# Performance work log

Hardware: AMD Instinct MI355X
Metric: run time of the kernel (lower is better)

## Reference

```python
import jax, jax.numpy as jnp
import numpy as np

D_MODEL = 1024
N_HEAD = 16
D_QKV = 64
B, L = 2, 2048
LN_EPS = 1e-5


def setup_inputs() -> dict:
    key = jax.random.key(0)
    ks = jax.random.split(key, 5)
    # xavier-normal-ish scale for [H, d_model, d_qkv] params
    std_in = (2.0 / (D_MODEL + D_QKV)) ** 0.5
    return {
        "x": jax.random.normal(ks[0], (B, L, D_MODEL), jnp.float32),
        "w_q": jax.random.normal(ks[1], (N_HEAD, D_MODEL, D_QKV), jnp.float32) * std_in,
        "w_k": jax.random.normal(ks[2], (N_HEAD, D_MODEL, D_QKV), jnp.float32) * std_in,
        "w_v": jax.random.normal(ks[3], (N_HEAD, D_MODEL, D_QKV), jnp.float32) * std_in,
        "w_o": jax.random.normal(ks[4], (N_HEAD, D_QKV, D_MODEL), jnp.float32) * std_in,
        "ln_gamma": jnp.ones((D_MODEL,), jnp.float32),
        "ln_beta": jnp.zeros((D_MODEL,), jnp.float32),
    }


def reference(x, w_q, w_k, w_v, w_o, ln_gamma, ln_beta):
    # q,k,v: [B, H, L, d_qkv]
    q = jnp.einsum('hmq,blm->bhlq', w_q, x)
    k = jnp.einsum('hmq,blm->bhlq', w_k, x)
    v = jnp.einsum('hmq,blm->bhlq', w_v, x)
    # scores: [B, H, L, L]
    s = jnp.einsum('bhiq,bhjq->bhij', q, k) / (D_QKV ** 0.5)
    s = jax.nn.softmax(s, axis=-1)
    # (dropout disabled: eval-mode reference)
    att = jnp.einsum('bhij,bhjq->bhiq', s, v)          # [B, H, L, d_qkv]
    out = jnp.einsum('bhlq,hqm->blm', att, w_o)        # [B, L, d_model]
    y = x + out                                        # residual
    mu = jnp.mean(y, axis=-1, keepdims=True)
    var = jnp.var(y, axis=-1, keepdims=True)
    return (y - mu) * jax.lax.rsqrt(var + LN_EPS) * ln_gamma + ln_beta
```

## Files before the change

### kernel.cpp

```cpp
#include <hip/hip_runtime.h>
#include <hip/hip_bf16.h>
#include <cstdint>

#define B_      2
#define L_      2048
#define DM_     1024
#define H_      16
#define DQ_     64
#define LN_EPS  1e-5f
#define QSCALE  0.1803368801111204f

typedef unsigned short u16;
typedef unsigned int   u32;
typedef __attribute__((ext_vector_type(8)))  short short8;
typedef __attribute__((ext_vector_type(4)))  unsigned short u16x4;
typedef __attribute__((ext_vector_type(4)))  unsigned int   u32x4;
typedef __attribute__((ext_vector_type(4)))  float f32x4;
typedef __attribute__((ext_vector_type(16))) float f32x16;

__device__ __forceinline__ u16 f2b(float f) {
  __hip_bfloat16 h = __float2bfloat16(f);
  return *reinterpret_cast<u16*>(&h);
}
__device__ __forceinline__ u32 pk2(float lo, float hi) {
  return (u32)f2b(lo) | ((u32)f2b(hi) << 16);
}

__device__ __forceinline__ void gl_lds16(const void* g, void* l) {
  auto gp = reinterpret_cast<const __attribute__((address_space(1))) unsigned int*>(
      reinterpret_cast<uintptr_t>(g));
  auto lp = reinterpret_cast<__attribute__((address_space(3))) unsigned int*>(
      reinterpret_cast<uintptr_t>(l));
  __builtin_amdgcn_global_load_lds(gp, lp, 16, 0, 0);
}

__device__ __forceinline__ short8 frag8(const u16* base, int row, int lchunk) {
  return *(const short8*)(base + row * 64 + ((lchunk ^ (row & 7)) << 3));
}

__global__ __launch_bounds__(256) void prep_all(
    const float* __restrict__ x, const float* __restrict__ wq,
    const float* __restrict__ wk, const float* __restrict__ wv,
    const float* __restrict__ wo, u16* __restrict__ xb,
    u16* __restrict__ wt, u16* __restrict__ wot) {
  __shared__ float Ls[64][65];
  const int t = threadIdx.x;
  const int bx = blockIdx.x;
  if (bx < 4096) {
    int i = bx * 256 + t;
    float4 v = ((const float4*)x)[i];
    u16x4 o = { f2b(v.x), f2b(v.y), f2b(v.z), f2b(v.w) };
    *(u16x4*)(xb + (size_t)i * 4) = o;
  } else if (bx < 4096 + 768) {
    int b2 = bx - 4096;
    int mt = b2 & 15, h = (b2 >> 4) & 15, wh = b2 >> 8;
    const float* in = ((wh == 0) ? wq : (wh == 1) ? wk : wv) + (size_t)h * DM_ * DQ_;
    #pragma unroll
    for (int i = 0; i < 16; ++i) {
      int idx = i * 256 + t, r = idx >> 6, c = idx & 63;
      Ls[r][c] = in[(size_t)(mt * 64 + r) * DQ_ + c];
    }
    __syncthreads();
    u16* outb = wt + (size_t)(wh * H_ + h) * DQ_ * DM_;
    #pragma unroll
    for (int i = 0; i < 16; ++i) {
      int idx = i * 256 + t, q = idx >> 6, mm = idx & 63;
      outb[(size_t)q * DM_ + mt * 64 + mm] = f2b(Ls[mm][q]);
    }
  } else {
    int b3 = bx - 4864;
    int mt = b3 & 15, kt = b3 >> 4;
    #pragma unroll
    for (int i = 0; i < 16; ++i) {
      int idx = i * 256 + t, r = idx >> 6, c = idx & 63;
      Ls[r][c] = wo[(size_t)(kt * 64 + r) * DM_ + mt * 64 + c];
    }
    __syncthreads();
    #pragma unroll
    for (int i = 0; i < 16; ++i) {
      int idx = i * 256 + t, mm = idx >> 6, kk = idx & 63;
      wot[(size_t)(mt * 64 + mm) * DM_ + kt * 64 + kk] = f2b(Ls[kk][mm]);
    }
  }
}

__global__ __launch_bounds__(256) void qkv_big(const u16* __restrict__ xb,
    const u16* __restrict__ wt, u16* __restrict__ Q, u16* __restrict__ K,
    u16* __restrict__ Vtg) {
  const int nt = blockIdx.x, mt = blockIdx.y;
  __shared__ __align__(16) u16 SH[128 * 136];
  u16* As_ = SH;
  u16* Bs_ = SH + 8192;
  const int t = threadIdx.x, w = t >> 6, lane = t & 63;
  const int lx = lane & 15, lq = lane >> 4;
  const int row0 = mt * 128, n0 = nt * 128;
  const int r8 = lane >> 3, lc = (lane & 7) ^ r8;
  const int wr = (w >> 1) * 64, wc = (w & 1) * 64;

  const u16* gA = xb + (size_t)(row0 + w * 32 + r8) * DM_ + lc * 8;
  const u16* gB = wt + (size_t)(n0  + w * 32 + r8) * DM_ + lc * 8;
  u16* lA = As_ + (w * 32) * 64;
  u16* lB = Bs_ + (w * 32) * 64;

  f32x4 z = {0.f, 0.f, 0.f, 0.f};
  f32x4 acc[4][4];
  #pragma unroll
  for (int mb = 0; mb < 4; ++mb)
    #pragma unroll
    for (int nb = 0; nb < 4; ++nb) acc[mb][nb] = z;

  for (int k0 = 0; k0 < DM_; k0 += 64) {
    #pragma unroll
    for (int i = 0; i < 4; ++i) {
      gl_lds16(gA + (size_t)i * 8 * DM_ + k0, lA + i * 8 * 64);
      gl_lds16(gB + (size_t)i * 8 * DM_ + k0, lB + i * 8 * 64);
    }
    __syncthreads();
    short8 af[4][2];
    #pragma unroll
    for (int mb = 0; mb < 4; ++mb)
      #pragma unroll
      for (int kh = 0; kh < 2; ++kh)
        af[mb][kh] = frag8(As_, wr + mb * 16 + lx, (kh << 2) | lq);
    #pragma unroll
    for (int nb = 0; nb < 4; ++nb) {
      short8 b0 = frag8(Bs_, wc + nb * 16 + lx, lq);
      short8 b1 = frag8(Bs_, wc + nb * 16 + lx, 4 | lq);
      #pragma unroll
      for (int mb = 0; mb < 4; ++mb) {
        acc[mb][nb] = __builtin_amdgcn_mfma_f32_16x16x32_bf16(af[mb][0], b0, acc[mb][nb], 0, 0, 0);
        acc[mb][nb] = __builtin_amdgcn_mfma_f32_16x16x32_bf16(af[mb][1], b1, acc[mb][nb], 0, 0, 0);
      }
    }
    __syncthreads();
  }

  const int wh = n0 >> 10;
  const float oscale = (wh == 0) ? QSCALE : 1.0f;
  const int bb = row0 >> 11, l0 = row0 & 2047;
  const int hd0 = n0 & 1023;
  u16* Ep = SH;

  if (wh != 2) {
    #pragma unroll
    for (int mb = 0; mb < 4; ++mb)
      #pragma unroll
      for (int nb = 0; nb < 4; ++nb)
        #pragma unroll
        for (int r = 0; r < 4; ++r) {
          int l = wr + mb * 16 + lq * 4 + r;
          Ep[l * 136 + wc + nb * 16 + lx] = f2b(acc[mb][nb][r] * oscale);
        }
    __syncthreads();
    u16* outp = (wh == 0) ? Q : K;
    #pragma unroll
    for (int hs = 0; hs < 2; ++hs) {
      const int hh = (hd0 >> 6) + hs;
      u16* gbase = outp + ((size_t)(bb * H_ + hh) * L_ + l0) * DQ_;
      #pragma unroll
      for (int it = 0; it < 4; ++it) {
        int u = it * 256 + t;
        int l = u >> 3, chunk = u & 7;
        *(uint4*)(gbase + u * 8) = *(const uint4*)&Ep[l * 136 + hs * 64 + chunk * 8];
      }
    }
  } else {
    #pragma unroll
    for (int mb = 0; mb < 4; ++mb)
      #pragma unroll
      for (int nb = 0; nb < 4; ++nb) {
        int l = wr + mb * 16 + lq * 4;
        int lp = (l & ~12) | ((l & 4) << 1) | ((l & 8) >> 1);
        uint2 pv = { pk2(acc[mb][nb][0], acc[mb][nb][1]),
                     pk2(acc[mb][nb][2], acc[mb][nb][3]) };
        *(uint2*)&Ep[(wc + nb * 16 + lx) * 136 + lp] = pv;
      }
    __syncthreads();
    #pragma unroll
    for (int it = 0; it < 8; ++it) {
      int v = it * 256 + t;
      int dloc = v >> 4, chunk = v & 15;
      int hh = (hd0 + dloc) >> 6, dd = (hd0 + dloc) & 63;
      u16* g = Vtg + ((size_t)(bb * H_ + hh) * DQ_ + dd) * L_ + l0 + chunk * 8;
      *(uint4*)g = *(const uint4*)&Ep[dloc * 136 + chunk * 8];
    }
  }
}

__global__ __launch_bounds__(512) void attn_mfma(const u16* __restrict__ Q,
    const u16* __restrict__ K, const u16* __restrict__ Vtg, u16* __restrict__ att) {
  const int qt = blockIdx.x, h = blockIdx.y, b = blockIdx.z;
  __shared__ __align__(16) u16 Qs_[256 * 64];
  __shared__ __align__(16) u16 Ks_[2][64 * 64];
  __shared__ __align__(16) u16 Vt_[2][64 * 64];
  const int t = threadIdx.x, w = t >> 6, lane = t & 63;
  const int c = lane & 31, lsel = lane >> 5;
  const int r8 = lane >> 3, lc = (lane & 7) ^ r8;
  const size_t bh  = (size_t)(b * H_ + h) * L_ * DQ_;
  const size_t bhv = (size_t)(b * H_ + h) * DQ_ * L_;

  const u16* gQ = Q + bh + (size_t)(qt * 256 + w * 32 + r8) * DQ_ + lc * 8;
  #pragma unroll
  for (int i = 0; i < 4; ++i) gl_lds16(gQ + (size_t)i * 8 * DQ_, Qs_ + (w * 32 + i * 8) * 64);

  const u16* gK = K   + bh  + (size_t)(w * 8 + r8) * DQ_ + lc * 8;
  const u16* gV = Vtg + bhv + (size_t)(w * 8 + r8) * L_  + lc * 8;

  gl_lds16(gK, Ks_[0] + w * 8 * 64);
  gl_lds16(gV, Vt_[0] + w * 8 * 64);
  __syncthreads();
  short8 qb[4];
  #pragma unroll
  for (int km = 0; km < 4; ++km) qb[km] = frag8(Qs_, w * 32 + c, (km << 1) | lsel);

  f32x16 zz = {0.f,0.f,0.f,0.f,0.f,0.f,0.f,0.f,0.f,0.f,0.f,0.f,0.f,0.f,0.f,0.f};
  f32x16 oacc0 = zz, oacc1 = zz, lacc = zz;
  const short one_bf = (short)0x3F80;
  short8 ones = {one_bf, one_bf, one_bf, one_bf, one_bf, one_bf, one_bf, one_bf};

  for (int kt = 0; kt < L_ / 64; ++kt) {
    const int cur = kt & 1;
    __syncthreads();

    if (kt + 1 < L_ / 64) {
      const int nxt = 1 - cur;
      gl_lds16(gK + (size_t)(kt + 1) * 64 * DQ_, Ks_[nxt] + w * 8 * 64);
      gl_lds16(gV + (size_t)(kt + 1) * 64,       Vt_[nxt] + w * 8 * 64);
    }

    u32x4 paw[4];
    #pragma unroll
    for (int kb = 0; kb < 2; ++kb) {
      f32x16 s = zz;
      #pragma unroll
      for (int km = 0; km < 4; ++km) {
        short8 ka = frag8(Ks_[cur], kb * 32 + c, (km << 1) | lsel);
        s = __builtin_amdgcn_mfma_f32_32x32x16_bf16(ka, qb[km], s, 0, 0, 0);
      }
      #pragma unroll
      for (int F = 0; F < 2; ++F) {
        u32x4 pw;
        #pragma unroll
        for (int i = 0; i < 4; ++i) {
          float p0 = __builtin_amdgcn_exp2f(s[8 * F + 2 * i]);
          float p1 = __builtin_amdgcn_exp2f(s[8 * F + 2 * i + 1]);
          pw[i] = __builtin_amdgcn_perm(__float_as_uint(p1), __float_as_uint(p0), 0x07060302u);
        }
        paw[2 * kb + F] = pw;
      }
    }

    #pragma unroll
    for (int km = 0; km < 4; ++km) {
      short8 pa  = *reinterpret_cast<const short8*>(&paw[km]);
      short8 vb0 = frag8(Vt_[cur], c,      (km << 1) | lsel);
      short8 vb1 = frag8(Vt_[cur], 32 + c, (km << 1) | lsel);
      oacc0 = __builtin_amdgcn_mfma_f32_32x32x16_bf16(pa, vb0, oacc0, 0, 0, 0);
      oacc1 = __builtin_amdgcn_mfma_f32_32x32x16_bf16(pa, vb1, oacc1, 0, 0, 0);
      lacc  = __builtin_amdgcn_mfma_f32_32x32x16_bf16(pa, ones, lacc, 0, 0, 0);
    }
  }

  const int qrow_base = qt * 256 + w * 32;
  #pragma unroll
  for (int r = 0; r < 16; ++r) {
    int qr = (r & 3) + 8 * (r >> 2) + 4 * lsel;
    float inv = 1.0f / lacc[r];
    size_t base = (size_t)(b * L_ + qrow_base + qr) * DM_ + h * DQ_;
    att[base + c]      = f2b(oacc0[r] * inv);
    att[base + 32 + c] = f2b(oacc1[r] * inv);
  }
}

__global__ __launch_bounds__(256) void oproj_big(const u16* __restrict__ A,
    const u16* __restrict__ wot, float* __restrict__ out) {
  const int nt = blockIdx.x, mt = blockIdx.y;
  __shared__ __align__(16) u16 As_[128 * 64];
  __shared__ __align__(16) u16 Bs_[64 * 64];
  const int t = threadIdx.x, w = t >> 6, lane = t & 63;
  const int lx = lane & 15, lq = lane >> 4;
  const int row0 = mt * 128, n0 = nt * 64;
  const int r8 = lane >> 3, lc = (lane & 7) ^ r8;

  const u16* gA = A   + (size_t)(row0 + w * 32 + r8) * DM_ + lc * 8;
  const u16* gB = wot + (size_t)(n0  + w * 16 + r8) * DM_ + lc * 8;
  u16* lA = As_ + (w * 32) * 64;
  u16* lB = Bs_ + (w * 16) * 64;

  f32x4 z = {0.f, 0.f, 0.f, 0.f};
  f32x4 acc[2][4];
  #pragma unroll
  for (int mb = 0; mb < 2; ++mb)
    #pragma unroll
    for (int nb = 0; nb < 4; ++nb) acc[mb][nb] = z;

  for (int k0 = 0; k0 < DM_; k0 += 64) {
    #pragma unroll
    for (int i = 0; i < 4; ++i)
      gl_lds16(gA + (size_t)i * 8 * DM_ + k0, lA + i * 8 * 64);
    #pragma unroll
    for (int i = 0; i < 2; ++i)
      gl_lds16(gB + (size_t)i * 8 * DM_ + k0, lB + i * 8 * 64);
    __syncthreads();
    short8 af[2][2];
    #pragma unroll
    for (int mb = 0; mb < 2; ++mb)
      #pragma unroll
      for (int kh = 0; kh < 2; ++kh)
        af[mb][kh] = frag8(As_, w * 32 + mb * 16 + lx, (kh << 2) | lq);
    #pragma unroll
    for (int nb = 0; nb < 4; ++nb) {
      short8 b0 = frag8(Bs_, nb * 16 + lx, lq);
      short8 b1 = frag8(Bs_, nb * 16 + lx, 4 | lq);
      acc[0][nb] = __builtin_amdgcn_mfma_f32_16x16x32_bf16(af[0][0], b0, acc[0][nb], 0, 0, 0);
      acc[0][nb] = __builtin_amdgcn_mfma_f32_16x16x32_bf16(af[0][1], b1, acc[0][nb], 0, 0, 0);
      acc[1][nb] = __builtin_amdgcn_mfma_f32_16x16x32_bf16(af[1][0], b0, acc[1][nb], 0, 0, 0);
      acc[1][nb] = __builtin_amdgcn_mfma_f32_16x16x32_bf16(af[1][1], b1, acc[1][nb], 0, 0, 0);
    }
    __syncthreads();
  }
  #pragma unroll
  for (int mb = 0; mb < 2; ++mb)
    #pragma unroll
    for (int nb = 0; nb < 4; ++nb)
      #pragma unroll
      for (int r = 0; r < 4; ++r) {
        int row = row0 + w * 32 + mb * 16 + lq * 4 + r;
        out[(size_t)row * DM_ + n0 + nb * 16 + lx] = acc[mb][nb][r];
      }
}

__global__ __launch_bounds__(256) void resid_ln(
    const float* __restrict__ x, const float* __restrict__ gamma,
    const float* __restrict__ beta, float* __restrict__ out) {
  const int row = blockIdx.x;
  const int t   = threadIdx.x;
  const float4* xp = (const float4*)(x   + (size_t)row * DM_);
  float4*       yp = (float4*)      (out + (size_t)row * DM_);

  float4 xv = xp[t];
  float4 av = yp[t];
  float y0 = xv.x + av.x, y1 = xv.y + av.y, y2 = xv.z + av.z, y3 = xv.w + av.w;

  float s  = y0 + y1 + y2 + y3;
  float s2 = y0 * y0 + y1 * y1 + y2 * y2 + y3 * y3;
  #pragma unroll
  for (int off = 32; off > 0; off >>= 1) {
    s  += __shfl_xor(s,  off, 64);
    s2 += __shfl_xor(s2, off, 64);
  }
  __shared__ float red[8];
  const int wave = t >> 6, lane = t & 63;
  if (lane == 0) { red[wave] = s; red[4 + wave] = s2; }
  __syncthreads();
  s  = red[0] + red[1] + red[2] + red[3];
  s2 = red[4] + red[5] + red[6] + red[7];

  const float mean = s * (1.f / DM_);
  const float var  = s2 * (1.f / DM_) - mean * mean;
  const float inv  = rsqrtf(var + LN_EPS);

  const float4 g  = ((const float4*)gamma)[t];
  const float4 bt = ((const float4*)beta)[t];
  float4 r;
  r.x = (y0 - mean) * inv * g.x + bt.x;
  r.y = (y1 - mean) * inv * g.y + bt.y;
  r.z = (y2 - mean) * inv * g.z + bt.z;
  r.w = (y3 - mean) * inv * g.w + bt.w;
  yp[t] = r;
}

extern "C" void kernel_launch(void* const* d_in, const int* in_sizes, int n_in,
                              void* d_out, int out_size, void* d_ws, size_t ws_size,
                              hipStream_t stream) {
  const float* x     = (const float*)d_in[0];
  const float* wq    = (const float*)d_in[1];
  const float* wk    = (const float*)d_in[2];
  const float* wv    = (const float*)d_in[3];
  const float* wo    = (const float*)d_in[4];
  const float* gamma = (const float*)d_in[5];
  const float* beta  = (const float*)d_in[6];
  float* out = (float*)d_out;

  char* ws = (char*)d_ws;
  u16* xb  = (u16*)ws;
  u16* Qb  = (u16*)(ws + ((size_t)8  << 20));
  u16* Kb  = (u16*)(ws + ((size_t)16 << 20));
  u16* Vtg = (u16*)(ws + ((size_t)24 << 20));
  u16* wt  = (u16*)(ws + ((size_t)32 << 20));
  u16* wot = (u16*)(ws + ((size_t)38 << 20));
  u16* att = (u16*)(ws + ((size_t)40 << 20));

  prep_all <<<5120, 256, 0, stream>>>(x, wq, wk, wv, wo, xb, wt, wot);
  qkv_big  <<<dim3(24, 32),    256, 0, stream>>>(xb, wt, Qb, Kb, Vtg);
  attn_mfma<<<dim3(L_ / 256, H_, B_), 512, 0, stream>>>(Qb, Kb, Vtg, att);
  oproj_big<<<dim3(16, 32),    256, 0, stream>>>(att, wot, out);
  resid_ln <<<B_ * L_, 256, 0, stream>>>(x, gamma, beta, out);
}
```

Before: 182.2 us.

## Halve attention block size and replace ones-MFMA row sum with VALU accumulation

The attention kernel now uses 128-query tiles with 4 waves instead of 256-query tiles with 8 waves. The grid doubles, and each wave loads two K/V rows per stage to cover the 64-row tile. The softmax denominator no longer comes from a third MFMA against a ones vector. Each lane instead sums its bf16-rounded probabilities, the two half-waves are combined with a shuffle, and the sums go through shared memory. This removes a third of the PV-stage MFMAs and a 16-register accumulator, at the cost of extra VALU adds and twice as much K/V traffic per query.

```diff
diff --git a/kernel.cpp b/kernel.cpp
--- a/kernel.cpp
+++ b/kernel.cpp
@@ -187,36 +187,38 @@
   }
 }
 
-__global__ __launch_bounds__(512) void attn_mfma(const u16* __restrict__ Q,
+__global__ __launch_bounds__(256) void attn_mfma(const u16* __restrict__ Q,
     const u16* __restrict__ K, const u16* __restrict__ Vtg, u16* __restrict__ att) {
   const int qt = blockIdx.x, h = blockIdx.y, b = blockIdx.z;
-  __shared__ __align__(16) u16 Qs_[256 * 64];
+  __shared__ __align__(16) u16 Qs_[128 * 64];
   __shared__ __align__(16) u16 Ks_[2][64 * 64];
   __shared__ __align__(16) u16 Vt_[2][64 * 64];
+  __shared__ float Qsum[4][32];
   const int t = threadIdx.x, w = t >> 6, lane = t & 63;
   const int c = lane & 31, lsel = lane >> 5;
   const int r8 = lane >> 3, lc = (lane & 7) ^ r8;
   const size_t bh  = (size_t)(b * H_ + h) * L_ * DQ_;
   const size_t bhv = (size_t)(b * H_ + h) * DQ_ * L_;
 
-  const u16* gQ = Q + bh + (size_t)(qt * 256 + w * 32 + r8) * DQ_ + lc * 8;
+  const u16* gQ = Q + bh + (size_t)(qt * 128 + w * 32 + r8) * DQ_ + lc * 8;
   #pragma unroll
   for (int i = 0; i < 4; ++i) gl_lds16(gQ + (size_t)i * 8 * DQ_, Qs_ + (w * 32 + i * 8) * 64);
 
-  const u16* gK = K   + bh  + (size_t)(w * 8 + r8) * DQ_ + lc * 8;
-  const u16* gV = Vtg + bhv + (size_t)(w * 8 + r8) * L_  + lc * 8;
-
-  gl_lds16(gK, Ks_[0] + w * 8 * 64);
-  gl_lds16(gV, Vt_[0] + w * 8 * 64);
+  const u16* gK = K   + bh  + (size_t)(w * 16 + r8) * DQ_ + lc * 8;
+  const u16* gV = Vtg + bhv + (size_t)(w * 16 + r8) * L_  + lc * 8;
+
+  gl_lds16(gK,                     Ks_[0] + (w * 16)     * 64);
+  gl_lds16(gK + (size_t)8 * DQ_,   Ks_[0] + (w * 16 + 8) * 64);
+  gl_lds16(gV,                     Vt_[0] + (w * 16)     * 64);
+  gl_lds16(gV + (size_t)8 * L_,    Vt_[0] + (w * 16 + 8) * 64);
   __syncthreads();
   short8 qb[4];
   #pragma unroll
   for (int km = 0; km < 4; ++km) qb[km] = frag8(Qs_, w * 32 + c, (km << 1) | lsel);
 
   f32x16 zz = {0.f,0.f,0.f,0.f,0.f,0.f,0.f,0.f,0.f,0.f,0.f,0.f,0.f,0.f,0.f,0.f};
-  f32x16 oacc0 = zz, oacc1 = zz, lacc = zz;
-  const short one_bf = (short)0x3F80;
-  short8 ones = {one_bf, one_bf, one_bf, one_bf, one_bf, one_bf, one_bf, one_bf};
+  f32x16 oacc0 = zz, oacc1 = zz;
+  float rsum = 0.f;
 
   for (int kt = 0; kt < L_ / 64; ++kt) {
     const int cur = kt & 1;
@@ -224,8 +226,10 @@
 
     if (kt + 1 < L_ / 64) {
       const int nxt = 1 - cur;
-      gl_lds16(gK + (size_t)(kt + 1) * 64 * DQ_, Ks_[nxt] + w * 8 * 64);
-      gl_lds16(gV + (size_t)(kt + 1) * 64,       Vt_[nxt] + w * 8 * 64);
+      gl_lds16(gK + (size_t)(kt + 1) * 64 * DQ_,                    Ks_[nxt] + (w * 16)     * 64);
+      gl_lds16(gK + (size_t)((kt + 1) * 64 + 8) * DQ_,              Ks_[nxt] + (w * 16 + 8) * 64);
+      gl_lds16(gV + (size_t)(kt + 1) * 64,                          Vt_[nxt] + (w * 16)     * 64);
+      gl_lds16(gV + (size_t)8 * L_ + (size_t)(kt + 1) * 64,         Vt_[nxt] + (w * 16 + 8) * 64);
     }
 
     u32x4 paw[4];
@@ -237,6 +241,7 @@
         short8 ka = frag8(Ks_[cur], kb * 32 + c, (km << 1) | lsel);
         s = __builtin_amdgcn_mfma_f32_32x32x16_bf16(ka, qb[km], s, 0, 0, 0);
       }
+      float tp[8];
       #pragma unroll
       for (int F = 0; F < 2; ++F) {
         u32x4 pw;
@@ -244,10 +249,15 @@
         for (int i = 0; i < 4; ++i) {
           float p0 = __builtin_amdgcn_exp2f(s[8 * F + 2 * i]);
           float p1 = __builtin_amdgcn_exp2f(s[8 * F + 2 * i + 1]);
-          pw[i] = __builtin_amdgcn_perm(__float_as_uint(p1), __float_as_uint(p0), 0x07060302u);
+          u32 pkd = __builtin_amdgcn_perm(__float_as_uint(p1), __float_as_uint(p0), 0x07060302u);
+          pw[i] = pkd;
+          float t0 = __uint_as_float(pkd << 16);
+          float t1 = __uint_as_float(pkd & 0xFFFF0000u);
+          tp[4 * F + i] = t0 + t1;
         }
         paw[2 * kb + F] = pw;
       }
+      rsum += ((tp[0] + tp[1]) + (tp[2] + tp[3])) + ((tp[4] + tp[5]) + (tp[6] + tp[7]));
     }
 
     #pragma unroll
@@ -257,15 +267,18 @@
       short8 vb1 = frag8(Vt_[cur], 32 + c, (km << 1) | lsel);
       oacc0 = __builtin_amdgcn_mfma_f32_32x32x16_bf16(pa, vb0, oacc0, 0, 0, 0);
       oacc1 = __builtin_amdgcn_mfma_f32_32x32x16_bf16(pa, vb1, oacc1, 0, 0, 0);
-      lacc  = __builtin_amdgcn_mfma_f32_32x32x16_bf16(pa, ones, lacc, 0, 0, 0);
-    }
-  }
-
-  const int qrow_base = qt * 256 + w * 32;
+    }
+  }
+
+  rsum += __shfl_xor(rsum, 32, 64);
+  if (lane < 32) Qsum[w][lane] = rsum;
+  __syncthreads();
+
+  const int qrow_base = qt * 128 + w * 32;
   #pragma unroll
   for (int r = 0; r < 16; ++r) {
     int qr = (r & 3) + 8 * (r >> 2) + 4 * lsel;
-    float inv = 1.0f / lacc[r];
+    float inv = 1.0f / Qsum[w][qr];
     size_t base = (size_t)(b * L_ + qrow_base + qr) * DM_ + h * DQ_;
     att[base + c]      = f2b(oacc0[r] * inv);
     att[base + 32 + c] = f2b(oacc1[r] * inv);
@@ -393,7 +406,7 @@
 
   prep_all <<<5120, 256, 0, stream>>>(x, wq, wk, wv, wo, xb, wt, wot);
   qkv_big  <<<dim3(24, 32),    256, 0, stream>>>(xb, wt, Qb, Kb, Vtg);
-  attn_mfma<<<dim3(L_ / 256, H_, B_), 512, 0, stream>>>(Qb, Kb, Vtg, att);
+  attn_mfma<<<dim3(L_ / 128, H_, B_), 256, 0, stream>>>(Qb, Kb, Vtg, att);
   oproj_big<<<dim3(16, 32),    256, 0, stream>>>(att, wot, out);
   resid_ln <<<B_ * L_, 256, 0, stream>>>(x, gamma, beta, out);
 }
```

New measurement: 193.6 us. 6.3% more time.
